# Kernel optimization log

Hardware: AMD Instinct MI355X
Metric: run time of the kernel (lower is better)

The kernel has to match this reference:

```python
import jax, jax.numpy as jnp
import numpy as np

N = 100000   # nodes
E = 100000   # hyperedges
M = 1600000  # incidences
IN_C = 128
HID = 128
OUT_C = 64
L = 2
EPS = 1e-5


def _layer_norm(x, g, b):
    m = jnp.mean(x, axis=-1, keepdims=True)
    v = jnp.mean((x - m) ** 2, axis=-1, keepdims=True)
    return (x - m) * jax.lax.rsqrt(v + EPS) * g + b


def setup_inputs() -> dict:
    key = jax.random.key(0)
    ks = jax.random.split(key, 16)
    s_in = 1.0 / np.sqrt(IN_C)
    s_h = 1.0 / np.sqrt(HID)
    return {
        "x": jax.random.normal(ks[0], (N, IN_C), jnp.float32),
        "x_e": jax.random.normal(ks[1], (E, IN_C), jnp.float32),
        "edge_index": jax.random.randint(ks[2], (2, M), 0, N, jnp.int32),
        "in_norm_g": jnp.ones((IN_C,), jnp.float32),
        "in_norm_b": jnp.zeros((IN_C,), jnp.float32),
        "in_proj_W": jax.random.normal(ks[3], (IN_C, HID), jnp.float32) * s_in,
        "in_proj_b": jnp.zeros((HID,), jnp.float32),
        "norm_g": jnp.ones((L, HID), jnp.float32),
        "norm_b": jnp.zeros((L, HID), jnp.float32),
        "conv_W": jax.random.normal(ks[4], (L, HID, HID), jnp.float32) * s_h,
        "conv_b": jnp.zeros((L, HID), jnp.float32),
        "lin_W": jax.random.normal(ks[5], (HID, OUT_C), jnp.float32) * s_h,
        "lin_b": jnp.zeros((OUT_C,), jnp.float32),
    }


def reference(x, x_e, edge_index, in_norm_g, in_norm_b, in_proj_W, in_proj_b,
              norm_g, norm_b, conv_W, conv_b, lin_W, lin_b):
    src, dst = edge_index[0], edge_index[1]  # node ids, hyperedge ids
    h = _layer_norm(x, in_norm_g, in_norm_b)
    h = jax.nn.leaky_relu(h @ in_proj_W + in_proj_b)  # dropout = identity (eval)

    # HypergraphConv degree normalizers (hyperedge_weight = 1)
    ones = jnp.ones((M,), h.dtype)
    degD = jax.ops.segment_sum(ones, src, num_segments=N)
    D = jnp.where(degD > 0, 1.0 / degD, 0.0)          # [N]
    degB = jax.ops.segment_sum(ones, dst, num_segments=E)
    B = jnp.where(degB > 0, 1.0 / degB, 0.0)          # [E]

    for i in range(L):
        hn = _layer_norm(h, norm_g[i], norm_b[i])
        xw = hn @ conv_W[i]                            # [N, HID]
        # node -> hyperedge: sum_j B[e] * xw[j]
        he = jax.ops.segment_sum(B[dst][:, None] * xw[src], dst, num_segments=E)
        # hyperedge -> node: sum_e D[n] * he[e]
        h2 = jax.ops.segment_sum(D[src][:, None] * he[dst], src, num_segments=N)
        h = jax.nn.leaky_relu(h2 + conv_b[i])

    # MinAggregation: segment-min of gathered node features per hyperedge
    agg = jax.ops.segment_min(h[src], dst, num_segments=E)  # [E, HID]
    return agg @ lin_W + lin_b                              # [E, OUT_C]
```

## Files before the change

kernel.cpp:

```cpp
#include <hip/hip_runtime.h>

#define NN 100000
#define NE 100000
#define MI 1600000
#define HID 128
#define OUTC 64
#define LSLOPE 0.01f
#define EPSV 1e-5f
#define ADJ_STRIDE 48

#define BUILD_PASSES 16
#define BUILD_WIN ((NN + BUILD_PASSES - 1) / BUILD_PASSES)
#define BUILD_ILP 4
#define BUILD_MB (256 * BUILD_ILP)
#define BUILD_NB ((MI + BUILD_MB - 1) / BUILD_MB)

typedef unsigned short us;
typedef __attribute__((ext_vector_type(4))) unsigned short us4;
typedef __attribute__((ext_vector_type(8))) unsigned short us8;
typedef __attribute__((ext_vector_type(8))) short short8;
typedef __attribute__((ext_vector_type(16))) float f32x16;

__device__ __forceinline__ float bf2f(us h) {
    return __uint_as_float(((unsigned)h) << 16);
}
__device__ __forceinline__ us f2bf(float f) {
    unsigned u = __float_as_uint(f);
    return (us)((u + 0x7FFFu + ((u >> 16) & 1u)) >> 16);
}

__global__ void build_all_kernel(const int* __restrict__ ei,
                                 int* __restrict__ cntE, int* __restrict__ cntN,
                                 int* __restrict__ adjE, int* __restrict__ adjN) {
    const int half = blockIdx.x / (8 * BUILD_NB);
    const int rem  = blockIdx.x - half * 8 * BUILD_NB;
    const int xcd  = rem & 7;
    const int mblk = rem >> 3;
    const int pass = half * 8 + xcd;
    const int lo = pass * BUILD_WIN;
    const int hi = lo + BUILD_WIN < NN ? lo + BUILD_WIN : NN;
    const int mbase = mblk * BUILD_MB + threadIdx.x;
    #pragma unroll
    for (int k = 0; k < BUILD_ILP; ++k) {
        int m = mbase + k * 256;
        if (m < MI) {
            int s = ei[m], d = ei[MI + m];
            if (d >= lo && d < hi) {
                int p = atomicAdd(&cntE[d], 1);
                if (p < ADJ_STRIDE) adjE[d * ADJ_STRIDE + p] = s;
            }
            if (s >= lo && s < hi) {
                int p = atomicAdd(&cntN[s], 1);
                if (p < ADJ_STRIDE) adjN[s * ADJ_STRIDE + p] = d;
            }
        }
    }
}

__global__ void prep_kernel(const int* __restrict__ cntE, const int* __restrict__ cntN,
                            float* __restrict__ B, float* __restrict__ D,
                            const float* __restrict__ in_W, const float* __restrict__ conv_W,
                            const float* __restrict__ lin_W,
                            us* __restrict__ wt_in, us* __restrict__ wt_c0,
                            us* __restrict__ wt_c1, us* __restrict__ wt_lin) {
    int i = blockIdx.x * blockDim.x + threadIdx.x;
    if (i < NE) {
        int d = cntE[i]; B[i] = d > 0 ? 1.0f / (float)d : 0.0f;
    } else if (i < NE + NN) {
        int j = i - NE;
        int d = cntN[j]; D[j] = d > 0 ? 1.0f / (float)d : 0.0f;
    } else {
        int idx = i - (NE + NN);
        if (idx < 49152) {
            int mat = idx >> 14, r = idx & 16383;
            const float* src = mat == 0 ? in_W : (mat == 1 ? conv_W : conv_W + 16384);
            us* dst = mat == 0 ? wt_in : (mat == 1 ? wt_c0 : wt_c1);
            int n = r >> 7, k = r & 127;
            dst[r] = f2bf(src[k * 128 + n]);
        } else if (idx < 57344) {
            int r = idx - 49152;
            int n = r >> 7, k = r & 127;
            float v = lin_W[k * 64 + n];
            us h = f2bf(v);
            wt_lin[r] = h;
            wt_lin[8192 + r] = f2bf(v - bf2f(h));
        }
    }
}

template <int MODE>
__global__ __launch_bounds__(256) void gather_kernel(
    const int* __restrict__ cnt, const int* __restrict__ adj,
    const us* __restrict__ src, const float* __restrict__ scale,
    const float* __restrict__ bias, us* __restrict__ dst, int R)
{
    const int q = threadIdx.x >> 4;
    const int lane = threadIdx.x & 15;
    const int r = blockIdx.x * 16 + q;
    if (r >= R) return;
    int n = cnt[r]; n = n < ADJ_STRIDE ? n : ADJ_STRIDE;
    const int* arow = adj + (size_t)r * ADJ_STRIDE;
    float a[8];
    #pragma unroll
    for (int k = 0; k < 8; ++k) a[k] = (MODE == 2) ? INFINITY : 0.f;
    const us* base = src + lane * 8;
    int j = 0;
    for (; j + 7 < n; j += 8) {
        us8 v[8];
        #pragma unroll
        for (int u = 0; u < 8; ++u)
            v[u] = *(const us8*)(base + (size_t)arow[j + u] * HID);
        #pragma unroll
        for (int u = 0; u < 8; ++u) {
            #pragma unroll
            for (int k = 0; k < 8; ++k) {
                float f = bf2f(v[u][k]);
                a[k] = (MODE == 2) ? fminf(a[k], f) : (a[k] + f);
            }
        }
    }
    for (; j < n; ++j) {
        us8 v = *(const us8*)(base + (size_t)arow[j] * HID);
        #pragma unroll
        for (int k = 0; k < 8; ++k) {
            float f = bf2f(v[k]);
            a[k] = (MODE == 2) ? fminf(a[k], f) : (a[k] + f);
        }
    }
    if (MODE == 0) {
        float s = scale[r];
        #pragma unroll
        for (int k = 0; k < 8; ++k) a[k] *= s;
    } else if (MODE == 1) {
        float s = scale[r];
        float4 b0 = *(const float4*)(bias + lane * 8);
        float4 b1 = *(const float4*)(bias + lane * 8 + 4);
        float bb[8] = {b0.x, b0.y, b0.z, b0.w, b1.x, b1.y, b1.z, b1.w};
        #pragma unroll
        for (int k = 0; k < 8; ++k) {
            float x = s * a[k] + bb[k];
            a[k] = x > 0.f ? x : LSLOPE * x;
        }
    }
    us8 o;
    #pragma unroll
    for (int k = 0; k < 8; ++k) o[k] = f2bf(a[k]);
    *(us8*)(dst + (size_t)r * HID + lane * 8) = o;
}

template <int NC, bool ABF16, bool OBF16, bool SPLIT>
__global__ __launch_bounds__(512) void mfma_gemm_kernel(
    const void* __restrict__ Av, const float* __restrict__ ln_g, const float* __restrict__ ln_b,
    const us* __restrict__ WT, const float* __restrict__ bias,
    void* __restrict__ outv, int R, int flags)
{
    constexpr int SA = 136;
    constexpr int NW = (SPLIT ? 2 : 1) * NC;
    constexpr int CT = NC / 64;
    __shared__ us As[128 * SA];
    __shared__ us Ws[NW * SA];
    __shared__ float red_s[512];
    __shared__ float red_q[512];
    __shared__ float r_mean[128];
    __shared__ float r_rstd[128];

    const int t = threadIdx.x;
    const int row0 = blockIdx.x * 128;

    constexpr int WUS4 = NW * 128 / 4;
    #pragma unroll
    for (int i = t; i < WUS4; i += 512) {
        us4 w = ((const us4*)WT)[i];
        int nrow = i >> 5, k4 = i & 31;
        *(us4*)(Ws + nrow * SA + k4 * 4) = w;
    }

    {
        const int r = t >> 2, sub = t & 3;
        const int gr = row0 + r;
        float v[32];
        if (gr < R) {
            if (ABF16) {
                const us* ap = (const us*)Av + (size_t)gr * 128 + sub * 32;
                #pragma unroll
                for (int j4 = 0; j4 < 8; ++j4) {
                    us4 x4 = *(const us4*)(ap + j4 * 4);
                    v[j4 * 4 + 0] = bf2f(x4.x); v[j4 * 4 + 1] = bf2f(x4.y);
                    v[j4 * 4 + 2] = bf2f(x4.z); v[j4 * 4 + 3] = bf2f(x4.w);
                }
            } else {
                const float* ap = (const float*)Av + (size_t)gr * 128 + sub * 32;
                #pragma unroll
                for (int j4 = 0; j4 < 8; ++j4) {
                    float4 f4 = *(const float4*)(ap + j4 * 4);
                    v[j4 * 4 + 0] = f4.x; v[j4 * 4 + 1] = f4.y;
                    v[j4 * 4 + 2] = f4.z; v[j4 * 4 + 3] = f4.w;
                }
            }
        } else {
            #pragma unroll
            for (int j = 0; j < 32; ++j) v[j] = 0.f;
        }
        if (flags & 1) {
            float s = 0.f, q = 0.f;
            #pragma unroll
            for (int j = 0; j < 32; ++j) { s += v[j]; q += v[j] * v[j]; }
            red_s[t] = s; red_q[t] = q;
            __syncthreads();
            if (t < 128) {
                float ss = red_s[t * 4] + red_s[t * 4 + 1] + red_s[t * 4 + 2] + red_s[t * 4 + 3];
                float qq = red_q[t * 4] + red_q[t * 4 + 1] + red_q[t * 4 + 2] + red_q[t * 4 + 3];
                float mu = ss * (1.0f / 128.0f);
                float var = qq * (1.0f / 128.0f) - mu * mu;
                r_mean[t] = mu;
                r_rstd[t] = rsqrtf(var + EPSV);
            }
            __syncthreads();
            float mu = r_mean[r], rs = r_rstd[r];
            #pragma unroll
            for (int j4 = 0; j4 < 8; ++j4) {
                float4 g4 = *(const float4*)(ln_g + sub * 32 + j4 * 4);
                float4 b4 = *(const float4*)(ln_b + sub * 32 + j4 * 4);
                v[j4 * 4 + 0] = (v[j4 * 4 + 0] - mu) * rs * g4.x + b4.x;
                v[j4 * 4 + 1] = (v[j4 * 4 + 1] - mu) * rs * g4.y + b4.y;
                v[j4 * 4 + 2] = (v[j4 * 4 + 2] - mu) * rs * g4.z + b4.z;
                v[j4 * 4 + 3] = (v[j4 * 4 + 3] - mu) * rs * g4.w + b4.w;
            }
        }
        #pragma unroll
        for (int j4 = 0; j4 < 8; ++j4) {
            us4 o;
            o.x = f2bf(v[j4 * 4 + 0]); o.y = f2bf(v[j4 * 4 + 1]);
            o.z = f2bf(v[j4 * 4 + 2]); o.w = f2bf(v[j4 * 4 + 3]);
            *(us4*)(As + r * SA + sub * 32 + j4 * 4) = o;
        }
    }
    __syncthreads();

    const int lane = t & 63;
    const int wave = t >> 6;
    const int wr = (wave & 3) * 32;
    const int wc = (wave >> 2) * (NC / 2);
    const int m = lane & 31;
    const int half = lane >> 5;
    const us* a_base = As + (wr + m) * SA + half * 8;

    f32x16 acc[CT];
    #pragma unroll
    for (int ct = 0; ct < CT; ++ct) acc[ct] = (f32x16)(0.0f);

    #pragma unroll
    for (int ks = 0; ks < 8; ++ks) {
        short8 a = *(const short8*)(a_base + ks * 16);
        #pragma unroll
        for (int ct = 0; ct < CT; ++ct) {
            const us* b_base = Ws + (wc + ct * 32 + m) * SA + half * 8 + ks * 16;
            short8 b = *(const short8*)b_base;
            acc[ct] = __builtin_amdgcn_mfma_f32_32x32x16_bf16(a, b, acc[ct], 0, 0, 0);
            if (SPLIT) {
                short8 bl = *(const short8*)(b_base + (size_t)NC * SA);
                acc[ct] = __builtin_amdgcn_mfma_f32_32x32x16_bf16(a, bl, acc[ct], 0, 0, 0);
            }
        }
    }

    #pragma unroll
    for (int ct = 0; ct < CT; ++ct) {
        int gc = wc + ct * 32 + m;
        float bv = bias ? bias[gc] : 0.f;
        #pragma unroll
        for (int reg = 0; reg < 16; ++reg) {
            int rloc = (reg & 3) + 8 * (reg >> 2) + 4 * half;
            int gr = row0 + wr + rloc;
            if (gr < R) {
                float y = acc[ct][reg] + bv;
                if (flags & 4) y = y > 0.f ? y : LSLOPE * y;
                if (OBF16) ((us*)outv)[(size_t)gr * NC + gc] = f2bf(y);
                else       ((float*)outv)[(size_t)gr * NC + gc] = y;
            }
        }
    }
}

extern "C" void kernel_launch(void* const* d_in, const int* in_sizes, int n_in,
                              void* d_out, int out_size, void* d_ws, size_t ws_size,
                              hipStream_t stream) {
    const float* x      = (const float*)d_in[0];
    const int*   ei     = (const int*)d_in[2];
    const float* in_g   = (const float*)d_in[3];
    const float* in_b   = (const float*)d_in[4];
    const float* in_W   = (const float*)d_in[5];
    const float* in_pb  = (const float*)d_in[6];
    const float* norm_g = (const float*)d_in[7];
    const float* norm_b = (const float*)d_in[8];
    const float* conv_W = (const float*)d_in[9];
    const float* conv_b = (const float*)d_in[10];
    const float* lin_W  = (const float*)d_in[11];
    const float* lin_b  = (const float*)d_in[12];
    float* out = (float*)d_out;

    us* h_bf   = (us*)d_ws;
    us* xw_bf  = h_bf  + (size_t)NN * HID;
    us* he_bf  = xw_bf + (size_t)NN * HID;
    us* agg_bf = he_bf + (size_t)NE * HID;
    float* D    = (float*)(agg_bf + (size_t)NE * HID);
    float* B    = D + NN;
    int* cntE   = (int*)(B + NE);
    int* cntN   = cntE + NE;
    int* adjE   = cntN + NN;
    int* adjN   = adjE + (size_t)NE * ADJ_STRIDE;
    us* wt_in  = (us*)(adjN + (size_t)NN * ADJ_STRIDE);
    us* wt_c0  = wt_in + 128 * 128;
    us* wt_c1  = wt_c0 + 128 * 128;
    us* wt_lin = wt_c1 + 128 * 128;

    hipMemsetAsync(cntE, 0, (size_t)(NN + NE) * sizeof(int), stream);
    build_all_kernel<<<BUILD_PASSES * BUILD_NB, 256, 0, stream>>>(ei, cntE, cntN, adjE, adjN);

    prep_kernel<<<(NE + NN + 57344 + 255) / 256, 256, 0, stream>>>(
        cntE, cntN, B, D, in_W, conv_W, lin_W, wt_in, wt_c0, wt_c1, wt_lin);

    mfma_gemm_kernel<HID, false, true, false><<<(NN + 127) / 128, 512, 0, stream>>>(
        x, in_g, in_b, wt_in, in_pb, h_bf, NN, 1 | 4);

    for (int i = 0; i < 2; ++i) {
        mfma_gemm_kernel<HID, true, true, false><<<(NN + 127) / 128, 512, 0, stream>>>(
            h_bf, norm_g + i * HID, norm_b + i * HID, i ? wt_c1 : wt_c0,
            nullptr, xw_bf, NN, 1);
        gather_kernel<0><<<(NE + 15) / 16, 256, 0, stream>>>(cntE, adjE, xw_bf, B, nullptr, he_bf, NE);
        gather_kernel<1><<<(NN + 15) / 16, 256, 0, stream>>>(cntN, adjN, he_bf, D, conv_b + i * HID, h_bf, NN);
    }

    gather_kernel<2><<<(NE + 15) / 16, 256, 0, stream>>>(cntE, adjE, h_bf, nullptr, nullptr, agg_bf, NE);

    mfma_gemm_kernel<OUTC, true, false, true><<<(NE + 127) / 128, 512, 0, stream>>>(
        agg_bf, nullptr, nullptr, wt_lin, lin_b, out, NE, 0);
}
```

Baseline: 735.0 us.

## Fuse min-aggregation with output linear, fold prep into build, inline degree scaling

The weight-conversion prep is merged into the adjacency build kernel, which now also reads eight incidences per thread with vector loads. The B/D reciprocal-degree arrays are dropped; the gather kernels compute 1/count inline. The segment-min gather and the final linear layer become one kernel that keeps each block's 16 min rows in LDS and applies split-bf16 16x16 MFMAs, avoiding the agg buffer round trip. Together these remove two launches and some global traffic, though the fused min kernel gets much less GEMM reuse per block.

```diff
diff --git a/kernel.cpp b/kernel.cpp
--- a/kernel.cpp
+++ b/kernel.cpp
@@ -11,14 +11,16 @@
 
 #define BUILD_PASSES 16
 #define BUILD_WIN ((NN + BUILD_PASSES - 1) / BUILD_PASSES)
-#define BUILD_ILP 4
+#define BUILD_ILP 8
 #define BUILD_MB (256 * BUILD_ILP)
 #define BUILD_NB ((MI + BUILD_MB - 1) / BUILD_MB)
+#define WPREP_NB 224
 
 typedef unsigned short us;
 typedef __attribute__((ext_vector_type(4))) unsigned short us4;
 typedef __attribute__((ext_vector_type(8))) unsigned short us8;
 typedef __attribute__((ext_vector_type(8))) short short8;
+typedef __attribute__((ext_vector_type(4))) float f32x4;
 typedef __attribute__((ext_vector_type(16))) float f32x16;
 
 __device__ __forceinline__ float bf2f(us h) {
@@ -29,55 +31,25 @@
     return (us)((u + 0x7FFFu + ((u >> 16) & 1u)) >> 16);
 }
 
-__global__ void build_all_kernel(const int* __restrict__ ei,
-                                 int* __restrict__ cntE, int* __restrict__ cntN,
-                                 int* __restrict__ adjE, int* __restrict__ adjN) {
-    const int half = blockIdx.x / (8 * BUILD_NB);
-    const int rem  = blockIdx.x - half * 8 * BUILD_NB;
-    const int xcd  = rem & 7;
-    const int mblk = rem >> 3;
-    const int pass = half * 8 + xcd;
-    const int lo = pass * BUILD_WIN;
-    const int hi = lo + BUILD_WIN < NN ? lo + BUILD_WIN : NN;
-    const int mbase = mblk * BUILD_MB + threadIdx.x;
-    #pragma unroll
-    for (int k = 0; k < BUILD_ILP; ++k) {
-        int m = mbase + k * 256;
-        if (m < MI) {
-            int s = ei[m], d = ei[MI + m];
-            if (d >= lo && d < hi) {
-                int p = atomicAdd(&cntE[d], 1);
-                if (p < ADJ_STRIDE) adjE[d * ADJ_STRIDE + p] = s;
-            }
-            if (s >= lo && s < hi) {
-                int p = atomicAdd(&cntN[s], 1);
-                if (p < ADJ_STRIDE) adjN[s * ADJ_STRIDE + p] = d;
-            }
-        }
-    }
-}
-
-__global__ void prep_kernel(const int* __restrict__ cntE, const int* __restrict__ cntN,
-                            float* __restrict__ B, float* __restrict__ D,
-                            const float* __restrict__ in_W, const float* __restrict__ conv_W,
-                            const float* __restrict__ lin_W,
-                            us* __restrict__ wt_in, us* __restrict__ wt_c0,
-                            us* __restrict__ wt_c1, us* __restrict__ wt_lin) {
-    int i = blockIdx.x * blockDim.x + threadIdx.x;
-    if (i < NE) {
-        int d = cntE[i]; B[i] = d > 0 ? 1.0f / (float)d : 0.0f;
-    } else if (i < NE + NN) {
-        int j = i - NE;
-        int d = cntN[j]; D[j] = d > 0 ? 1.0f / (float)d : 0.0f;
-    } else {
-        int idx = i - (NE + NN);
+__global__ __launch_bounds__(256) void build_all_kernel(
+    const int* __restrict__ ei,
+    int* __restrict__ cntE, int* __restrict__ cntN,
+    int* __restrict__ adjE, int* __restrict__ adjN,
+    const float* __restrict__ in_W, const float* __restrict__ conv_W,
+    const float* __restrict__ lin_W,
+    us* __restrict__ wt_in, us* __restrict__ wt_c0,
+    us* __restrict__ wt_c1, us* __restrict__ wt_lin)
+{
+    const int t = threadIdx.x;
+    if (blockIdx.x < WPREP_NB) {
+        int idx = blockIdx.x * 256 + t;
         if (idx < 49152) {
             int mat = idx >> 14, r = idx & 16383;
             const float* src = mat == 0 ? in_W : (mat == 1 ? conv_W : conv_W + 16384);
             us* dst = mat == 0 ? wt_in : (mat == 1 ? wt_c0 : wt_c1);
             int n = r >> 7, k = r & 127;
             dst[r] = f2bf(src[k * 128 + n]);
-        } else if (idx < 57344) {
+        } else {
             int r = idx - 49152;
             int n = r >> 7, k = r & 127;
             float v = lin_W[k * 64 + n];
@@ -85,24 +57,54 @@
             wt_lin[r] = h;
             wt_lin[8192 + r] = f2bf(v - bf2f(h));
         }
+        return;
+    }
+    const int local = blockIdx.x - WPREP_NB;
+    const int half = local / (8 * BUILD_NB);
+    const int rem  = local - half * 8 * BUILD_NB;
+    const int xcd  = rem & 7;
+    const int mblk = rem >> 3;
+    const int pass = half * 8 + xcd;
+    const int lo = pass * BUILD_WIN;
+    const int hi = lo + BUILD_WIN < NN ? lo + BUILD_WIN : NN;
+    const int m0 = mblk * BUILD_MB + t * 8;
+    if (m0 >= MI) return;
+    int4 sa = *(const int4*)(ei + m0);
+    int4 sb = *(const int4*)(ei + m0 + 4);
+    int4 da = *(const int4*)(ei + MI + m0);
+    int4 db = *(const int4*)(ei + MI + m0 + 4);
+    int ss[8] = {sa.x, sa.y, sa.z, sa.w, sb.x, sb.y, sb.z, sb.w};
+    int dd[8] = {da.x, da.y, da.z, da.w, db.x, db.y, db.z, db.w};
+    #pragma unroll
+    for (int k = 0; k < 8; ++k) {
+        int s = ss[k], d = dd[k];
+        if (d >= lo && d < hi) {
+            int p = atomicAdd(&cntE[d], 1);
+            if (p < ADJ_STRIDE) adjE[d * ADJ_STRIDE + p] = s;
+        }
+        if (s >= lo && s < hi) {
+            int p = atomicAdd(&cntN[s], 1);
+            if (p < ADJ_STRIDE) adjN[s * ADJ_STRIDE + p] = d;
+        }
     }
 }
 
 template <int MODE>
 __global__ __launch_bounds__(256) void gather_kernel(
     const int* __restrict__ cnt, const int* __restrict__ adj,
-    const us* __restrict__ src, const float* __restrict__ scale,
-    const float* __restrict__ bias, us* __restrict__ dst, int R)
+    const us* __restrict__ src, const float* __restrict__ bias,
+    us* __restrict__ dst, int R)
 {
     const int q = threadIdx.x >> 4;
     const int lane = threadIdx.x & 15;
     const int r = blockIdx.x * 16 + q;
     if (r >= R) return;
-    int n = cnt[r]; n = n < ADJ_STRIDE ? n : ADJ_STRIDE;
+    const int nraw = cnt[r];
+    int n = nraw < ADJ_STRIDE ? nraw : ADJ_STRIDE;
     const int* arow = adj + (size_t)r * ADJ_STRIDE;
     float a[8];
     #pragma unroll
-    for (int k = 0; k < 8; ++k) a[k] = (MODE == 2) ? INFINITY : 0.f;
+    for (int k = 0; k < 8; ++k) a[k] = 0.f;
     const us* base = src + lane * 8;
     int j = 0;
     for (; j + 7 < n; j += 8) {
@@ -113,26 +115,19 @@
         #pragma unroll
         for (int u = 0; u < 8; ++u) {
             #pragma unroll
-            for (int k = 0; k < 8; ++k) {
-                float f = bf2f(v[u][k]);
-                a[k] = (MODE == 2) ? fminf(a[k], f) : (a[k] + f);
-            }
+            for (int k = 0; k < 8; ++k) a[k] += bf2f(v[u][k]);
         }
     }
     for (; j < n; ++j) {
         us8 v = *(const us8*)(base + (size_t)arow[j] * HID);
         #pragma unroll
-        for (int k = 0; k < 8; ++k) {
-            float f = bf2f(v[k]);
-            a[k] = (MODE == 2) ? fminf(a[k], f) : (a[k] + f);
-        }
-    }
+        for (int k = 0; k < 8; ++k) a[k] += bf2f(v[k]);
+    }
+    float s = nraw > 0 ? 1.0f / (float)nraw : 0.f;
     if (MODE == 0) {
-        float s = scale[r];
         #pragma unroll
         for (int k = 0; k < 8; ++k) a[k] *= s;
-    } else if (MODE == 1) {
-        float s = scale[r];
+    } else {
         float4 b0 = *(const float4*)(bias + lane * 8);
         float4 b1 = *(const float4*)(bias + lane * 8 + 4);
         float bb[8] = {b0.x, b0.y, b0.z, b0.w, b1.x, b1.y, b1.z, b1.w};
@@ -148,17 +143,81 @@
     *(us8*)(dst + (size_t)r * HID + lane * 8) = o;
 }
 
-template <int NC, bool ABF16, bool OBF16, bool SPLIT>
+__global__ __launch_bounds__(256) void min_lin_kernel(
+    const int* __restrict__ cnt, const int* __restrict__ adj,
+    const us* __restrict__ src, const us* __restrict__ wt_lin,
+    const float* __restrict__ lin_b, float* __restrict__ out)
+{
+    __shared__ us Amin[16 * 136];
+    const int t = threadIdx.x;
+    {
+        const int q = t >> 4;
+        const int lane = t & 15;
+        const int r = blockIdx.x * 16 + q;
+        const int nraw = cnt[r];
+        int n = nraw < ADJ_STRIDE ? nraw : ADJ_STRIDE;
+        const int* arow = adj + (size_t)r * ADJ_STRIDE;
+        float a[8];
+        #pragma unroll
+        for (int k = 0; k < 8; ++k) a[k] = INFINITY;
+        const us* base = src + lane * 8;
+        int j = 0;
+        for (; j + 7 < n; j += 8) {
+            us8 v[8];
+            #pragma unroll
+            for (int u = 0; u < 8; ++u)
+                v[u] = *(const us8*)(base + (size_t)arow[j + u] * HID);
+            #pragma unroll
+            for (int u = 0; u < 8; ++u) {
+                #pragma unroll
+                for (int k = 0; k < 8; ++k) a[k] = fminf(a[k], bf2f(v[u][k]));
+            }
+        }
+        for (; j < n; ++j) {
+            us8 v = *(const us8*)(base + (size_t)arow[j] * HID);
+            #pragma unroll
+            for (int k = 0; k < 8; ++k) a[k] = fminf(a[k], bf2f(v[k]));
+        }
+        us8 o;
+        #pragma unroll
+        for (int k = 0; k < 8; ++k) o[k] = f2bf(a[k]);
+        *(us8*)(Amin + q * 136 + lane * 8) = o;
+    }
+    __syncthreads();
+    const int l = t & 63;
+    const int w = t >> 6;
+    const int cr = l & 15;
+    const int ko = (l >> 4) * 8;
+    f32x4 acc = {0.f, 0.f, 0.f, 0.f};
+    const us* Wb = wt_lin + (size_t)(w * 16 + cr) * 128 + ko;
+    const us* Ab = Amin + cr * 136 + ko;
+    #pragma unroll
+    for (int ks = 0; ks < 4; ++ks) {
+        short8 a  = *(const short8*)(Ab + ks * 32);
+        short8 bh = *(const short8*)(Wb + ks * 32);
+        short8 bl = *(const short8*)(Wb + 8192 + ks * 32);
+        acc = __builtin_amdgcn_mfma_f32_16x16x32_bf16(a, bh, acc, 0, 0, 0);
+        acc = __builtin_amdgcn_mfma_f32_16x16x32_bf16(a, bl, acc, 0, 0, 0);
+    }
+    const int gc = w * 16 + cr;
+    const float bv = lin_b[gc];
+    const int r0 = blockIdx.x * 16 + (l >> 4) * 4;
+    #pragma unroll
+    for (int j = 0; j < 4; ++j) {
+        out[(size_t)(r0 + j) * OUTC + gc] = acc[j] + bv;
+    }
+}
+
+template <int NC, bool ABF16, bool OBF16>
 __global__ __launch_bounds__(512) void mfma_gemm_kernel(
     const void* __restrict__ Av, const float* __restrict__ ln_g, const float* __restrict__ ln_b,
     const us* __restrict__ WT, const float* __restrict__ bias,
     void* __restrict__ outv, int R, int flags)
 {
     constexpr int SA = 136;
-    constexpr int NW = (SPLIT ? 2 : 1) * NC;
     constexpr int CT = NC / 64;
     __shared__ us As[128 * SA];
-    __shared__ us Ws[NW * SA];
+    __shared__ us Ws[NC * SA];
     __shared__ float red_s[512];
     __shared__ float red_q[512];
     __shared__ float r_mean[128];
@@ -167,7 +226,7 @@
     const int t = threadIdx.x;
     const int row0 = blockIdx.x * 128;
 
-    constexpr int WUS4 = NW * 128 / 4;
+    constexpr int WUS4 = NC * 128 / 4;
     #pragma unroll
     for (int i = t; i < WUS4; i += 512) {
         us4 w = ((const us4*)WT)[i];
@@ -257,10 +316,6 @@
             const us* b_base = Ws + (wc + ct * 32 + m) * SA + half * 8 + ks * 16;
             short8 b = *(const short8*)b_base;
             acc[ct] = __builtin_amdgcn_mfma_f32_32x32x16_bf16(a, b, acc[ct], 0, 0, 0);
-            if (SPLIT) {
-                short8 bl = *(const short8*)(b_base + (size_t)NC * SA);
-                acc[ct] = __builtin_amdgcn_mfma_f32_32x32x16_bf16(a, bl, acc[ct], 0, 0, 0);
-            }
         }
     }
 
@@ -302,10 +357,7 @@
     us* h_bf   = (us*)d_ws;
     us* xw_bf  = h_bf  + (size_t)NN * HID;
     us* he_bf  = xw_bf + (size_t)NN * HID;
-    us* agg_bf = he_bf + (size_t)NE * HID;
-    float* D    = (float*)(agg_bf + (size_t)NE * HID);
-    float* B    = D + NN;
-    int* cntE   = (int*)(B + NE);
+    int* cntE   = (int*)(he_bf + (size_t)NE * HID);
     int* cntN   = cntE + NE;
     int* adjE   = cntN + NN;
     int* adjN   = adjE + (size_t)NE * ADJ_STRIDE;
@@ -315,24 +367,19 @@
     us* wt_lin = wt_c1 + 128 * 128;
 
     hipMemsetAsync(cntE, 0, (size_t)(NN + NE) * sizeof(int), stream);
-    build_all_kernel<<<BUILD_PASSES * BUILD_NB, 256, 0, stream>>>(ei, cntE, cntN, adjE, adjN);
-
-    prep_kernel<<<(NE + NN + 57344 + 255) / 256, 256, 0, stream>>>(
-        cntE, cntN, B, D, in_W, conv_W, lin_W, wt_in, wt_c0, wt_c1, wt_lin);
-
-    mfma_gemm_kernel<HID, false, true, false><<<(NN + 127) / 128, 512, 0, stream>>>(
+    build_all_kernel<<<WPREP_NB + BUILD_PASSES * BUILD_NB, 256, 0, stream>>>(
+        ei, cntE, cntN, adjE, adjN, in_W, conv_W, lin_W, wt_in, wt_c0, wt_c1, wt_lin);
+
+    mfma_gemm_kernel<HID, false, true><<<(NN + 127) / 128, 512, 0, stream>>>(
         x, in_g, in_b, wt_in, in_pb, h_bf, NN, 1 | 4);
 
     for (int i = 0; i < 2; ++i) {
-        mfma_gemm_kernel<HID, true, true, false><<<(NN + 127) / 128, 512, 0, stream>>>(
+        mfma_gemm_kernel<HID, true, true><<<(NN + 127) / 128, 512, 0, stream>>>(
             h_bf, norm_g + i * HID, norm_b + i * HID, i ? wt_c1 : wt_c0,
             nullptr, xw_bf, NN, 1);
-        gather_kernel<0><<<(NE + 15) / 16, 256, 0, stream>>>(cntE, adjE, xw_bf, B, nullptr, he_bf, NE);
-        gather_kernel<1><<<(NN + 15) / 16, 256, 0, stream>>>(cntN, adjN, he_bf, D, conv_b + i * HID, h_bf, NN);
-    }
-
-    gather_kernel<2><<<(NE + 15) / 16, 256, 0, stream>>>(cntE, adjE, h_bf, nullptr, nullptr, agg_bf, NE);
-
-    mfma_gemm_kernel<OUTC, true, false, true><<<(NE + 127) / 128, 512, 0, stream>>>(
-        agg_bf, nullptr, nullptr, wt_lin, lin_b, out, NE, 0);
-}
+        gather_kernel<0><<<(NE + 15) / 16, 256, 0, stream>>>(cntE, adjE, xw_bf, nullptr, he_bf, NE);
+        gather_kernel<1><<<(NN + 15) / 16, 256, 0, stream>>>(cntN, adjN, he_bf, conv_b + i * HID, h_bf, NN);
+    }
+
+    min_lin_kernel<<<NE / 16, 256, 0, stream>>>(cntE, adjE, h_bf, wt_lin, lin_b, out);
+}
```

After: 725.5 us. Within noise of the previous version (-1.3%).
